# Performance work log

Hardware: AMD Instinct MI355X
Metric: run time of the kernel (lower is better)

Reference implementation:

```python
import jax, jax.numpy as jnp
import numpy as np

HIDDEN = 1024
HEADS = 16
HEAD_DIM = HIDDEN // HEADS
POS_DIM = 128
B, S = 2, 2048
ROPE_BASE = 10000.0


def setup_inputs() -> dict:
    key = jax.random.key(0)
    ks = jax.random.split(key, 8)
    sd = 1.0 / np.sqrt(HIDDEN)
    return {
        "x":   jax.random.normal(ks[0], (B, S, HIDDEN), dtype=jnp.float32),
        "W_q": jax.random.normal(ks[1], (HIDDEN, HIDDEN), dtype=jnp.float32) * sd,
        "W_k": jax.random.normal(ks[2], (HIDDEN, HIDDEN), dtype=jnp.float32) * sd,
        "W_v": jax.random.normal(ks[3], (HIDDEN, HIDDEN), dtype=jnp.float32) * sd,
        "W_o": jax.random.normal(ks[4], (HIDDEN, HIDDEN), dtype=jnp.float32) * sd,
        "repo_W1": jax.random.normal(ks[5], (HIDDEN, POS_DIM), dtype=jnp.float32) * sd,
        "repo_b1": jnp.zeros((POS_DIM,), dtype=jnp.float32),
        "repo_W2": jax.random.normal(ks[6], (POS_DIM, 1), dtype=jnp.float32) * (1.0 / np.sqrt(POS_DIM)),
        "repo_b2": jnp.zeros((1,), dtype=jnp.float32),
    }


def _repo_positions(x, W1, b1, W2, b2):
    # 2-layer MLP -> scalar per token; softplus + cumsum gives monotone learned positions
    h = jax.nn.gelu(jnp.einsum("bsd,dp->bsp", x, W1) + b1)
    raw = (jnp.einsum("bsp,po->bso", h, W2) + b2)[..., 0]      # (B, S)
    return jnp.cumsum(jax.nn.softplus(raw), axis=1)             # (B, S)


def _apply_rope(q, k, positions):
    # q, k: (B, S, H, Dh); positions: (B, S) continuous
    half = HEAD_DIM // 2
    inv_freq = 1.0 / (ROPE_BASE ** (jnp.arange(0, HEAD_DIM, 2, dtype=jnp.float32) / HEAD_DIM))
    angles = positions[:, :, None] * inv_freq                   # (B, S, half)
    cos = jnp.cos(angles)[:, :, None, :]                        # (B, S, 1, half)
    sin = jnp.sin(angles)[:, :, None, :]

    def rot(t):
        t1, t2 = t[..., :half], t[..., half:]
        return jnp.concatenate([t1 * cos - t2 * sin, t1 * sin + t2 * cos], axis=-1)

    return rot(q), rot(k)


def reference(x, W_q, W_k, W_v, W_o, repo_W1, repo_b1, repo_W2, repo_b2):
    scale = 1.0 / np.sqrt(HEAD_DIM)
    q = jnp.einsum("bsd,de->bse", x, W_q).reshape(B, S, HEADS, HEAD_DIM)
    k = jnp.einsum("bsd,de->bse", x, W_k).reshape(B, S, HEADS, HEAD_DIM)
    v = jnp.einsum("bsd,de->bse", x, W_v).reshape(B, S, HEADS, HEAD_DIM)

    positions = _repo_positions(x, repo_W1, repo_b1, repo_W2, repo_b2)
    q, k = _apply_rope(q, k, positions)

    # explicit O(S^2) attention, matching the torch module
    scores = jnp.einsum("bqhd,bkhd->bhqk", q, k) * scale        # (B, H, S, S)
    attn = jax.nn.softmax(scores, axis=-1)
    out = jnp.einsum("bhqk,bkhd->bqhd", attn, v)                # (B, S, H, Dh)
    out = out.reshape(B, S, HIDDEN)
    return jnp.einsum("bsd,de->bse", out, W_o)
```

## Files before the change

### kernel.cpp

```cpp
#include <hip/hip_runtime.h>
#include <hip/hip_bf16.h>
#include <math.h>

#define HIDDEN 1024
#define HEADS 16
#define HEAD_DIM 64
#define POS_DIM 128
#define BATCH 2
#define SEQ 2048
#define TOKENS (BATCH * SEQ)

typedef _Float16 f16;
typedef __attribute__((ext_vector_type(8))) _Float16 f16x8;
typedef __attribute__((ext_vector_type(4))) _Float16 f16x4;
typedef __attribute__((ext_vector_type(4))) float f32x4;

__device__ __forceinline__ void glds16(const f16* g, f16* l) {
    __builtin_amdgcn_global_load_lds((const __attribute__((address_space(1))) unsigned int*)g,
                                     (__attribute__((address_space(3))) unsigned int*)l, 16, 0, 0);
}

__global__ __launch_bounds__(256) void cast_x_kernel(const float* __restrict__ x,
                                                     f16* __restrict__ o) {
    const int i = (blockIdx.x * 256 + threadIdx.x) * 8;
    const float4 u = *(const float4*)(x + i);
    const float4 v = *(const float4*)(x + i + 4);
    f16x8 r = {(f16)u.x, (f16)u.y, (f16)u.z, (f16)u.w,
               (f16)v.x, (f16)v.y, (f16)v.z, (f16)v.w};
    *(f16x8*)(o + i) = r;
}

__global__ __launch_bounds__(256) void cast_wt4_kernel(const float* __restrict__ W0,
                                                       const float* __restrict__ W1,
                                                       const float* __restrict__ W2,
                                                       const float* __restrict__ W3,
                                                       f16* __restrict__ Wt) {
    __shared__ float ts[32][33];
    const int t = threadIdx.x;
    const int z = blockIdx.z;
    const float* W = (z == 0) ? W0 : (z == 1) ? W1 : (z == 2) ? W2 : W3;
    f16* dst = Wt + (size_t)z * HIDDEN * HIDDEN;
    const int k0 = blockIdx.y * 32, n0 = blockIdx.x * 32;
    {
        const int r = t >> 3, c4 = (t & 7) * 4;
        const float4 u = *(const float4*)(W + (size_t)(k0 + r) * HIDDEN + n0 + c4);
        ts[r][c4 + 0] = u.x; ts[r][c4 + 1] = u.y; ts[r][c4 + 2] = u.z; ts[r][c4 + 3] = u.w;
    }
    __syncthreads();
    {
        const int r = t >> 3, c4 = (t & 7) * 4;
        f16* o = dst + (size_t)(n0 + r) * HIDDEN + k0 + c4;
        o[0] = (f16)ts[c4 + 0][r]; o[1] = (f16)ts[c4 + 1][r];
        o[2] = (f16)ts[c4 + 2][r]; o[3] = (f16)ts[c4 + 3][r];
    }
}

__global__ __launch_bounds__(256) void cast_w1t_kernel(const float* __restrict__ W1,
                                                       f16* __restrict__ Wh,
                                                       f16* __restrict__ Wl) {
    __shared__ float ts[32][33];
    const int t = threadIdx.x;
    const int k0 = blockIdx.y * 32, p0 = blockIdx.x * 32;
    {
        const int r = t >> 3, c4 = (t & 7) * 4;
        const float4 u = *(const float4*)(W1 + (size_t)(k0 + r) * POS_DIM + p0 + c4);
        ts[r][c4 + 0] = u.x; ts[r][c4 + 1] = u.y; ts[r][c4 + 2] = u.z; ts[r][c4 + 3] = u.w;
    }
    __syncthreads();
    {
        const int r = t >> 3, c4 = (t & 7) * 4;
        f16* oh = Wh + (size_t)(p0 + r) * HIDDEN + k0 + c4;
        f16* ol = Wl + (size_t)(p0 + r) * HIDDEN + k0 + c4;
#pragma unroll
        for (int u = 0; u < 4; ++u) {
            const float v = ts[c4 + u][r];
            const f16 hi = (f16)v;
            oh[u] = hi;
            ol[u] = (f16)(v - (float)hi);
        }
    }
}

__global__ __launch_bounds__(256, 3) void gemm_gll(const f16* __restrict__ A,
                                                   const f16* __restrict__ Bt,
                                                   f16* __restrict__ Cb,
                                                   float* __restrict__ Cf,
                                                   int N, int f16out) {
    __shared__ __align__(16) f16 As[128 * 64];
    __shared__ __align__(16) f16 Bs[128 * 64];
    const int tid = threadIdx.x;
    const int w = tid >> 6, lane = tid & 63;
    const int g = lane >> 4, c = lane & 15;
    const int m0 = blockIdx.y * 128, n0 = blockIdx.x * 128;
    const int wm = (w & 1) * 64, wn = (w >> 1) * 64;

    const int lrow = lane >> 3;
    const int lseg = (lane & 7) ^ lrow;
    const f16* gA = A + (size_t)(m0 + w * 32 + lrow) * 1024 + lseg * 8;
    const f16* gB = Bt + (size_t)(n0 + w * 32 + lrow) * 1024 + lseg * 8;
    f16* lA = &As[(w * 32) * 64];
    f16* lB = &Bs[(w * 32) * 64];

    f32x4 acc[4][4];
    const f32x4 z = {0.f, 0.f, 0.f, 0.f};
#pragma unroll
    for (int i = 0; i < 4; ++i)
#pragma unroll
        for (int j = 0; j < 4; ++j) acc[i][j] = z;

    const int rsw = c & 7;
    for (int k0 = 0; k0 < 1024; k0 += 64) {
        __syncthreads();
#pragma unroll
        for (int p = 0; p < 4; ++p) {
            glds16(gA + (size_t)p * 8 * 1024 + k0, lA + p * 8 * 64);
            glds16(gB + (size_t)p * 8 * 1024 + k0, lB + p * 8 * 64);
        }
        __syncthreads();
#pragma unroll
        for (int s = 0; s < 2; ++s) {
            f16x8 af[4], bf[4];
#pragma unroll
            for (int i = 0; i < 4; ++i)
                af[i] = *(const f16x8*)&As[(wm + i * 16 + c) * 64 + (((s * 4 + g) ^ rsw) * 8)];
#pragma unroll
            for (int j = 0; j < 4; ++j)
                bf[j] = *(const f16x8*)&Bs[(wn + j * 16 + c) * 64 + (((s * 4 + g) ^ rsw) * 8)];
#pragma unroll
            for (int i = 0; i < 4; ++i)
#pragma unroll
                for (int j = 0; j < 4; ++j)
                    acc[i][j] = __builtin_amdgcn_mfma_f32_16x16x32_f16(af[i], bf[j], acc[i][j], 0, 0, 0);
        }
    }
#pragma unroll
    for (int i = 0; i < 4; ++i)
#pragma unroll
        for (int j = 0; j < 4; ++j)
#pragma unroll
            for (int r = 0; r < 4; ++r) {
                const size_t off = (size_t)(m0 + wm + i * 16 + 4 * g + r) * N + n0 + wn + j * 16 + c;
                if (f16out) Cb[off] = (f16)acc[i][j][r];
                else Cf[off] = acc[i][j][r];
            }
}

__device__ __forceinline__ float gelu_tanh(float x) {
    const float kA = 0.7978845608028654f;
    return 0.5f * x * (1.0f + tanhf(kA * (x + 0.044715f * x * x * x)));
}

__global__ __launch_bounds__(256, 2) void repo_mfma(const float* __restrict__ x,
                                                    const f16* __restrict__ w1h,
                                                    const f16* __restrict__ w1l,
                                                    const float* __restrict__ b1,
                                                    const float* __restrict__ W2,
                                                    const float* __restrict__ b2,
                                                    float* __restrict__ raw) {
    __shared__ __align__(16) f16 Ash[64 * 32], Asl[64 * 32];
    __shared__ __align__(16) f16 Bsh[128 * 32], Bsl[128 * 32];
    __shared__ float red[4][64];
    const int tid = threadIdx.x;
    const int w = tid >> 6, lane = tid & 63;
    const int g = lane >> 4, c = lane & 15;
    const int m0 = blockIdx.x * 64;

    const int arow = tid >> 2, aseg = tid & 3;
    const int aslot = (aseg ^ ((arow ^ (arow >> 2)) & 3)) << 3;
    const float* gA = x + (size_t)(m0 + arow) * 1024 + aseg * 8;
    const f16* gBh0 = w1h + (size_t)arow * 1024 + aseg * 8;
    const f16* gBh1 = w1h + (size_t)(arow + 64) * 1024 + aseg * 8;
    const f16* gBl0 = w1l + (size_t)arow * 1024 + aseg * 8;
    const f16* gBl1 = w1l + (size_t)(arow + 64) * 1024 + aseg * 8;
    f16* sAh = &Ash[arow * 32 + aslot];
    f16* sAl = &Asl[arow * 32 + aslot];
    f16* sBh0 = &Bsh[arow * 32 + aslot];
    f16* sBh1 = &Bsh[(arow + 64) * 32 + aslot];
    f16* sBl0 = &Bsl[arow * 32 + aslot];
    f16* sBl1 = &Bsl[(arow + 64) * 32 + aslot];

    const int foff = ((g ^ ((c ^ (c >> 2)) & 3)) << 3);

    f32x4 acc[4][2];
    const f32x4 z = {0.f, 0.f, 0.f, 0.f};
#pragma unroll
    for (int i = 0; i < 4; ++i) { acc[i][0] = z; acc[i][1] = z; }

    float4 pa0 = *(const float4*)gA;
    float4 pa1 = *(const float4*)(gA + 4);
    f16x8 pbh0 = *(const f16x8*)gBh0, pbh1 = *(const f16x8*)gBh1;
    f16x8 pbl0 = *(const f16x8*)gBl0, pbl1 = *(const f16x8*)gBl1;

    for (int k0 = 0; k0 < 1024; k0 += 32) {
        __syncthreads();
        {
            const float av[8] = {pa0.x, pa0.y, pa0.z, pa0.w, pa1.x, pa1.y, pa1.z, pa1.w};
            f16x8 ah, al;
#pragma unroll
            for (int u = 0; u < 8; ++u) {
                const f16 hi = (f16)av[u];
                ah[u] = hi;
                al[u] = (f16)(av[u] - (float)hi);
            }
            *(f16x8*)sAh = ah; *(f16x8*)sAl = al;
            *(f16x8*)sBh0 = pbh0; *(f16x8*)sBh1 = pbh1;
            *(f16x8*)sBl0 = pbl0; *(f16x8*)sBl1 = pbl1;
        }
        __syncthreads();
        if (k0 + 32 < 1024) {
            pa0 = *(const float4*)(gA + k0 + 32);
            pa1 = *(const float4*)(gA + k0 + 36);
            pbh0 = *(const f16x8*)(gBh0 + k0 + 32);
            pbh1 = *(const f16x8*)(gBh1 + k0 + 32);
            pbl0 = *(const f16x8*)(gBl0 + k0 + 32);
            pbl1 = *(const f16x8*)(gBl1 + k0 + 32);
        }
        f16x8 ah[4], al[4], bh[2], bl[2];
#pragma unroll
        for (int i = 0; i < 4; ++i) {
            ah[i] = *(const f16x8*)&Ash[(i * 16 + c) * 32 + foff];
            al[i] = *(const f16x8*)&Asl[(i * 16 + c) * 32 + foff];
        }
#pragma unroll
        for (int j = 0; j < 2; ++j) {
            bh[j] = *(const f16x8*)&Bsh[(w * 32 + j * 16 + c) * 32 + foff];
            bl[j] = *(const f16x8*)&Bsl[(w * 32 + j * 16 + c) * 32 + foff];
        }
#pragma unroll
        for (int i = 0; i < 4; ++i)
#pragma unroll
            for (int j = 0; j < 2; ++j) {
                acc[i][j] = __builtin_amdgcn_mfma_f32_16x16x32_f16(ah[i], bh[j], acc[i][j], 0, 0, 0);
                acc[i][j] = __builtin_amdgcn_mfma_f32_16x16x32_f16(ah[i], bl[j], acc[i][j], 0, 0, 0);
                acc[i][j] = __builtin_amdgcn_mfma_f32_16x16x32_f16(al[i], bh[j], acc[i][j], 0, 0, 0);
            }
    }
    float b1v[2], w2v[2];
#pragma unroll
    for (int j = 0; j < 2; ++j) {
        const int col = w * 32 + j * 16 + c;
        b1v[j] = b1[col];
        w2v[j] = W2[col];
    }
    float part[4][4];
#pragma unroll
    for (int i = 0; i < 4; ++i)
#pragma unroll
        for (int r = 0; r < 4; ++r) {
            float s = 0.f;
#pragma unroll
            for (int j = 0; j < 2; ++j)
                s += gelu_tanh(acc[i][j][r] + b1v[j]) * w2v[j];
            s += __shfl_xor(s, 1, 64);
            s += __shfl_xor(s, 2, 64);
            s += __shfl_xor(s, 4, 64);
            s += __shfl_xor(s, 8, 64);
            part[i][r] = s;
        }
    if (c == 0)
#pragma unroll
        for (int i = 0; i < 4; ++i)
#pragma unroll
            for (int r = 0; r < 4; ++r)
                red[w][i * 16 + 4 * g + r] = part[i][r];
    __syncthreads();
    if (tid < 64)
        raw[m0 + tid] = red[0][tid] + red[1][tid] + red[2][tid] + red[3][tid] + b2[0];
}

__device__ __forceinline__ double softplus_d(double x) {
    return (x > 0.0) ? x + log1p(exp(-x)) : log1p(exp(x));
}

__global__ __launch_bounds__(256) void repo_cumsum_kernel(const float* __restrict__ raw,
                                                          float* __restrict__ pos) {
    __shared__ double bufA[256];
    __shared__ double bufB[256];
    const int b = blockIdx.x;
    const int t = threadIdx.x;
    const float* r = raw + (size_t)b * SEQ;

    double loc[8];
    double sum = 0.0;
#pragma unroll
    for (int i = 0; i < 8; ++i) {
        sum += softplus_d((double)r[t * 8 + i]);
        loc[i] = sum;
    }
    bufA[t] = sum;
    __syncthreads();

    double* src = bufA;
    double* dst = bufB;
    for (int off = 1; off < 256; off <<= 1) {
        double v = src[t];
        if (t >= off) v += src[t - off];
        dst[t] = v;
        __syncthreads();
        double* tmp = src; src = dst; dst = tmp;
    }
    const double excl = src[t] - sum;
#pragma unroll
    for (int i = 0; i < 8; ++i)
        pos[(size_t)b * SEQ + t * 8 + i] = (float)(excl + loc[i]);
}

__global__ __launch_bounds__(256) void sctab_kernel(const float* __restrict__ pos,
                                                    float* __restrict__ costab,
                                                    float* __restrict__ sintab) {
    const int idx = blockIdx.x * 256 + threadIdx.x;
    const int tok = idx >> 5, i = idx & 31;
    const double ang = (double)pos[tok] * exp(-(double)i * 0.28782313662425574);
    double sa, ca;
    sincos(ang, &sa, &ca);
    costab[idx] = (float)ca;
    sintab[idx] = (float)sa;
}

__global__ __launch_bounds__(256) void packkv_kernel(f16* __restrict__ qkv,
                                                     const float* __restrict__ costab,
                                                     const float* __restrict__ sintab,
                                                     f16* __restrict__ kfo,
                                                     f16* __restrict__ vfo) {
    __shared__ __align__(16) f16 kds[64][72];
    __shared__ __align__(16) f16 vds[64][72];
    const int t = threadIdx.x;
    const int s0 = blockIdx.x * 64;
    const int h = blockIdx.y, b = blockIdx.z;
    const int key = t >> 2, part = t & 3;
    const int tok = b * SEQ + s0 + key;
    {
        float cs[8], sn[8];
        *(float4*)cs       = *(const float4*)(costab + tok * 32 + part * 8);
        *(float4*)(cs + 4) = *(const float4*)(costab + tok * 32 + part * 8 + 4);
        *(float4*)sn       = *(const float4*)(sintab + tok * 32 + part * 8);
        *(float4*)(sn + 4) = *(const float4*)(sintab + tok * 32 + part * 8 + 4);
        f16* qrow = qkv + (size_t)tok * 3072 + h * HEAD_DIM;
        {
            f16x8 lo = *(const f16x8*)(qrow + part * 8);
            f16x8 hi = *(const f16x8*)(qrow + part * 8 + 32);
#pragma unroll
            for (int u = 0; u < 8; ++u) {
                const float l = (float)lo[u], hh = (float)hi[u];
                lo[u] = (f16)(l * cs[u] - hh * sn[u]);
                hi[u] = (f16)(l * sn[u] + hh * cs[u]);
            }
            *(f16x8*)(qrow + part * 8) = lo;
            *(f16x8*)(qrow + part * 8 + 32) = hi;
        }
        const f16* krow = qrow + 1024;
        {
            f16x8 lo = *(const f16x8*)(krow + part * 8);
            f16x8 hi = *(const f16x8*)(krow + part * 8 + 32);
#pragma unroll
            for (int u = 0; u < 8; ++u) {
                const float l = (float)lo[u], hh = (float)hi[u];
                kds[key][part * 8 + u]      = (f16)(l * cs[u] - hh * sn[u]);
                kds[key][32 + part * 8 + u] = (f16)(l * sn[u] + hh * cs[u]);
            }
        }
        const f16* vrow = qrow + 2048;
        f16x8 v0 = *(const f16x8*)(vrow + part * 16);
        f16x8 v1 = *(const f16x8*)(vrow + part * 16 + 8);
#pragma unroll
        for (int u = 0; u < 8; ++u) {
            vds[part * 16 + u][key] = v0[u];
            vds[part * 16 + 8 + u][key] = v1[u];
        }
    }
    __syncthreads();
    const size_t cb = ((size_t)((b * HEADS + h) * 32) + blockIdx.x) * 4096;
#pragma unroll
    for (int p = 0; p < 2; ++p) {
        const int idx = p * 256 + t;
        const int frag = idx >> 6, lane = idx & 63;
        const int jn = frag >> 1, half = frag & 1, g = lane >> 4, c = lane & 15;
        *(f16x8*)(kfo + cb + frag * 512 + lane * 8) =
            *(const f16x8*)(&kds[jn * 16 + c][half * 32 + g * 8]);
    }
#pragma unroll
    for (int p = 0; p < 4; ++p) {
        const int idx = p * 256 + t;
        const int frag = idx >> 6, lane = idx & 63;
        const int jd = frag >> 2, jn = frag & 3, g = lane >> 4, c = lane & 15;
        *(f16x4*)(vfo + cb + frag * 256 + lane * 4) =
            *(const f16x4*)(&vds[jd * 16 + c][jn * 16 + 4 * g]);
    }
}

__global__ __launch_bounds__(256, 2) void attn_f16(const f16* __restrict__ qkv,
                                                   const f16* __restrict__ kfr,
                                                   const f16* __restrict__ vfr,
                                                   f16* __restrict__ aof0,
                                                   f16* __restrict__ aof1,
                                                   float* __restrict__ lsb) {
    __shared__ __align__(16) f16 kls[4096];
    __shared__ __align__(16) f16 vls[4096];
    __shared__ __align__(16) f16 ot[4][32][72];
    const int tid = threadIdx.x;
    const int w = tid >> 6, lane = tid & 63;
    const int g = lane >> 4, c = lane & 15;
    const int h = blockIdx.y;
    const int b = blockIdx.z >> 1, half = blockIdx.z & 1;
    const int bh = b * HEADS + h;
    const int row0 = blockIdx.x * 128 + w * 32;
    const int ch0 = half * 16;

    const f16* qb = qkv + (size_t)(b * SEQ + row0) * 3072 + h * HEAD_DIM + g * 8;
    const f16* kfb = kfr + (size_t)bh * 32 * 4096;
    const f16* vfb = vfr + (size_t)bh * 32 * 4096;

    f16x8 qf[2][2];
#pragma unroll
    for (int i = 0; i < 2; ++i) {
        qf[i][0] = *(const f16x8*)(qb + (size_t)(i * 16 + c) * 3072);
        qf[i][1] = *(const f16x8*)(qb + (size_t)(i * 16 + c) * 3072 + 32);
    }
    const f32x4 z = {0.f, 0.f, 0.f, 0.f};
    f32x4 acc[4][2];
    f32x4 accl[2];
#pragma unroll
    for (int jd = 0; jd < 4; ++jd) { acc[jd][0] = z; acc[jd][1] = z; }
    accl[0] = z; accl[1] = z;

    const f16x4 ones = {(f16)1.f, (f16)1.f, (f16)1.f, (f16)1.f};
    const float SC = 0.125f * 1.4426950408889634f;

    for (int cc = 0; cc < 16; ++cc) {
        const int ch = ch0 + cc;
        __syncthreads();
        {
            const f16* kg = kfb + (size_t)ch * 4096 + w * 1024 + lane * 8;
            const f16* vg = vfb + (size_t)ch * 4096 + w * 1024 + lane * 8;
            glds16(kg, kls + w * 1024);
            glds16(kg + 512, kls + w * 1024 + 512);
            glds16(vg, vls + w * 1024);
            glds16(vg + 512, vls + w * 1024 + 512);
        }
        __syncthreads();

        f16x8 kf[8];
        f16x4 vf[16];
#pragma unroll
        for (int f = 0; f < 8; ++f) kf[f] = *(const f16x8*)(kls + lane * 8 + f * 512);
#pragma unroll
        for (int f = 0; f < 16; ++f) vf[f] = *(const f16x4*)(vls + lane * 4 + f * 256);

#pragma unroll
        for (int i = 0; i < 2; ++i) {
            f32x4 s[4];
#pragma unroll
            for (int jn = 0; jn < 4; ++jn) {
                s[jn] = __builtin_amdgcn_mfma_f32_16x16x32_f16(kf[jn * 2], qf[i][0], z, 0, 0, 0);
                s[jn] = __builtin_amdgcn_mfma_f32_16x16x32_f16(kf[jn * 2 + 1], qf[i][1], s[jn], 0, 0, 0);
            }
#pragma unroll
            for (int jn = 0; jn < 4; ++jn) {
                f16x4 pf;
#pragma unroll
                for (int r = 0; r < 4; ++r)
                    pf[r] = (f16)__builtin_amdgcn_exp2f(fmaf(s[jn][r], SC, -8.0f));
                accl[i] = __builtin_amdgcn_mfma_f32_16x16x16f16(ones, pf, accl[i], 0, 0, 0);
#pragma unroll
                for (int jd = 0; jd < 4; ++jd)
                    acc[jd][i] = __builtin_amdgcn_mfma_f32_16x16x16f16(vf[jd * 4 + jn], pf, acc[jd][i], 0, 0, 0);
            }
        }
    }

    if (lane < 16) {
#pragma unroll
        for (int i = 0; i < 2; ++i)
            lsb[((size_t)(half * 32 + bh)) * SEQ + row0 + i * 16 + lane] = accl[i][0];
    }
#pragma unroll
    for (int i = 0; i < 2; ++i)
#pragma unroll
        for (int jd = 0; jd < 4; ++jd)
#pragma unroll
            for (int r = 0; r < 4; ++r)
                ot[w][i * 16 + c][jd * 16 + 4 * g + r] = (f16)acc[jd][i][r];
    f16* aofH = half ? aof1 : aof0;
    const int tr = lane >> 1, hf = lane & 1;
    f16* aob = aofH + (size_t)(b * SEQ + row0 + tr) * HIDDEN + h * HEAD_DIM + hf * 32;
#pragma unroll
    for (int q = 0; q < 4; ++q)
        *(f16x8*)(aob + q * 8) = *(const f16x8*)(&ot[w][tr][hf * 32 + q * 8]);
}

__global__ __launch_bounds__(256) void combine_kernel(f16* __restrict__ a0,
                                                      const f16* __restrict__ a1,
                                                      const float* __restrict__ lsb) {
    const int idx = blockIdx.x * 256 + threadIdx.x;
    const int part = idx & 127;
    const int tok = idx >> 7;
    const int h = part >> 3, d8 = (part & 7) * 8;
    const int b = tok >> 11, s = tok & 2047;
    const size_t li = (size_t)(b * HEADS + h) * SEQ + s;
    const float inv = 1.0f / (lsb[li] + lsb[32 * SEQ + li]);
    const size_t off = (size_t)tok * HIDDEN + h * HEAD_DIM + d8;
    const f16x8 u = *(const f16x8*)(a0 + off);
    const f16x8 v = *(const f16x8*)(a1 + off);
    f16x8 o;
#pragma unroll
    for (int q = 0; q < 8; ++q) o[q] = (f16)(((float)u[q] + (float)v[q]) * inv);
    *(f16x8*)(a0 + off) = o;
}

extern "C" void kernel_launch(void* const* d_in, const int* in_sizes, int n_in,
                              void* d_out, int out_size, void* d_ws, size_t ws_size,
                              hipStream_t stream) {
    const float* x   = (const float*)d_in[0];
    const float* W_q = (const float*)d_in[1];
    const float* W_k = (const float*)d_in[2];
    const float* W_v = (const float*)d_in[3];
    const float* W_o = (const float*)d_in[4];
    const float* rW1 = (const float*)d_in[5];
    const float* rb1 = (const float*)d_in[6];
    const float* rW2 = (const float*)d_in[7];
    const float* rb2 = (const float*)d_in[8];
    float* out = (float*)d_out;

    const size_t MAT = (size_t)TOKENS * HIDDEN;
    const size_t WSZ = (size_t)HIDDEN * HIDDEN;
    f16* x16  = (f16*)d_ws;
    f16* wqkv = x16 + MAT;
    f16* wot  = wqkv + 3 * WSZ;
    f16* qkv  = wot + WSZ;
    f16* kfr  = qkv + 3 * MAT;
    f16* vfr  = kfr + MAT;
    f16* aof0 = vfr + MAT;
    f16* aof1 = aof0 + MAT;
    f16* w1h  = aof1 + MAT;
    f16* w1l  = w1h + POS_DIM * HIDDEN;
    float* raw    = (float*)(w1l + POS_DIM * HIDDEN);
    float* pos    = raw + TOKENS;
    float* costab = pos + TOKENS;
    float* sintab = costab + TOKENS * 32;
    float* lsb    = sintab + TOKENS * 32;

    cast_x_kernel<<<MAT / 2048, 256, 0, stream>>>(x, x16);
    cast_wt4_kernel<<<dim3(32, 32, 4), 256, 0, stream>>>(W_q, W_k, W_v, W_o, wqkv);
    cast_w1t_kernel<<<dim3(4, 32), 256, 0, stream>>>(rW1, w1h, w1l);

    gemm_gll<<<dim3(24, 32), 256, 0, stream>>>(x16, wqkv, qkv, nullptr, 3072, 1);

    repo_mfma<<<64, 256, 0, stream>>>(x, w1h, w1l, rb1, rW2, rb2, raw);
    repo_cumsum_kernel<<<BATCH, 256, 0, stream>>>(raw, pos);
    sctab_kernel<<<TOKENS * 32 / 256, 256, 0, stream>>>(pos, costab, sintab);

    packkv_kernel<<<dim3(SEQ / 64, HEADS, BATCH), 256, 0, stream>>>(qkv, costab, sintab, kfr, vfr);

    attn_f16<<<dim3(SEQ / 128, HEADS, BATCH * 2), 256, 0, stream>>>(qkv, kfr, vfr, aof0, aof1, lsb);
    combine_kernel<<<TOKENS * 128 / 256, 256, 0, stream>>>(aof0, aof1, lsb);

    gemm_gll<<<dim3(8, 32), 256, 0, stream>>>(aof0, wot, nullptr, out, 1024, 0);
}
```

Baseline: 252.9 us.

## Double-buffer K/V chunk loads in attention and raise occupancy hint

The attention kernel now prefetches the next K/V chunk into an alternate LDS buffer with global_load_lds while computing on the current one. It waits with a partial vmcnt and a raw s_barrier instead of two __syncthreads per iteration. The separate K, V and output LDS arrays are merged into one 32KB region that is reused for the output transpose, and launch_bounds is raised to 4 blocks per CU. This hides global-load latency behind MFMA work, at the cost of more LDS per block and tighter register limits from the higher occupancy target.

```diff
diff --git a/kernel.cpp b/kernel.cpp
--- a/kernel.cpp
+++ b/kernel.cpp
@@ -388,15 +388,13 @@
     }
 }
 
-__global__ __launch_bounds__(256, 2) void attn_f16(const f16* __restrict__ qkv,
+__global__ __launch_bounds__(256, 4) void attn_f16(const f16* __restrict__ qkv,
                                                    const f16* __restrict__ kfr,
                                                    const f16* __restrict__ vfr,
                                                    f16* __restrict__ aof0,
                                                    f16* __restrict__ aof1,
                                                    float* __restrict__ lsb) {
-    __shared__ __align__(16) f16 kls[4096];
-    __shared__ __align__(16) f16 vls[4096];
-    __shared__ __align__(16) f16 ot[4][32][72];
+    __shared__ __align__(16) f16 smem[16384];
     const int tid = threadIdx.x;
     const int w = tid >> 6, lane = tid & 63;
     const int g = lane >> 4, c = lane & 15;
@@ -407,8 +405,8 @@
     const int ch0 = half * 16;
 
     const f16* qb = qkv + (size_t)(b * SEQ + row0) * 3072 + h * HEAD_DIM + g * 8;
-    const f16* kfb = kfr + (size_t)bh * 32 * 4096;
-    const f16* vfb = vfr + (size_t)bh * 32 * 4096;
+    const f16* kfb = kfr + (size_t)bh * 32 * 4096 + (size_t)ch0 * 4096;
+    const f16* vfb = vfr + (size_t)bh * 32 * 4096 + (size_t)ch0 * 4096;
 
     f16x8 qf[2][2];
 #pragma unroll
@@ -426,25 +424,38 @@
     const f16x4 ones = {(f16)1.f, (f16)1.f, (f16)1.f, (f16)1.f};
     const float SC = 0.125f * 1.4426950408889634f;
 
+    {
+        const f16* kg = kfb + w * 1024 + lane * 8;
+        const f16* vg = vfb + w * 1024 + lane * 8;
+        glds16(kg, smem + w * 1024);
+        glds16(kg + 512, smem + w * 1024 + 512);
+        glds16(vg, smem + 8192 + w * 1024);
+        glds16(vg + 512, smem + 8192 + w * 1024 + 512);
+    }
+
     for (int cc = 0; cc < 16; ++cc) {
-        const int ch = ch0 + cc;
-        __syncthreads();
         {
-            const f16* kg = kfb + (size_t)ch * 4096 + w * 1024 + lane * 8;
-            const f16* vg = vfb + (size_t)ch * 4096 + w * 1024 + lane * 8;
-            glds16(kg, kls + w * 1024);
-            glds16(kg + 512, kls + w * 1024 + 512);
-            glds16(vg, vls + w * 1024);
-            glds16(vg + 512, vls + w * 1024 + 512);
-        }
-        __syncthreads();
-
+            const int nc = (cc + 1 < 16) ? cc + 1 : 15;
+            const int nb = (cc + 1) & 1;
+            const f16* kg = kfb + (size_t)nc * 4096 + w * 1024 + lane * 8;
+            const f16* vg = vfb + (size_t)nc * 4096 + w * 1024 + lane * 8;
+            glds16(kg, smem + nb * 4096 + w * 1024);
+            glds16(kg + 512, smem + nb * 4096 + w * 1024 + 512);
+            glds16(vg, smem + 8192 + nb * 4096 + w * 1024);
+            glds16(vg + 512, smem + 8192 + nb * 4096 + w * 1024 + 512);
+        }
+        asm volatile("s_waitcnt vmcnt(4)" ::: "memory");
+        __builtin_amdgcn_s_barrier();
+        asm volatile("" ::: "memory");
+
+        const f16* kb = smem + (cc & 1) * 4096;
+        const f16* vb = smem + 8192 + (cc & 1) * 4096;
         f16x8 kf[8];
         f16x4 vf[16];
 #pragma unroll
-        for (int f = 0; f < 8; ++f) kf[f] = *(const f16x8*)(kls + lane * 8 + f * 512);
-#pragma unroll
-        for (int f = 0; f < 16; ++f) vf[f] = *(const f16x4*)(vls + lane * 4 + f * 256);
+        for (int f = 0; f < 8; ++f) kf[f] = *(const f16x8*)(kb + lane * 8 + f * 512);
+#pragma unroll
+        for (int f = 0; f < 16; ++f) vf[f] = *(const f16x4*)(vb + lane * 4 + f * 256);
 
 #pragma unroll
         for (int i = 0; i < 2; ++i) {
@@ -466,7 +477,10 @@
                     acc[jd][i] = __builtin_amdgcn_mfma_f32_16x16x16f16(vf[jd * 4 + jn], pf, acc[jd][i], 0, 0, 0);
             }
         }
-    }
+        asm volatile("" ::: "memory");
+        __builtin_amdgcn_s_barrier();
+    }
+    __syncthreads();
 
     if (lane < 16) {
 #pragma unroll
@@ -479,13 +493,13 @@
         for (int jd = 0; jd < 4; ++jd)
 #pragma unroll
             for (int r = 0; r < 4; ++r)
-                ot[w][i * 16 + c][jd * 16 + 4 * g + r] = (f16)acc[jd][i][r];
+                smem[(w * 32 + i * 16 + c) * 72 + jd * 16 + 4 * g + r] = (f16)acc[jd][i][r];
     f16* aofH = half ? aof1 : aof0;
     const int tr = lane >> 1, hf = lane & 1;
     f16* aob = aofH + (size_t)(b * SEQ + row0 + tr) * HIDDEN + h * HEAD_DIM + hf * 32;
 #pragma unroll
     for (int q = 0; q < 4; ++q)
-        *(f16x8*)(aob + q * 8) = *(const f16x8*)(&ot[w][tr][hf * 32 + q * 8]);
+        *(f16x8*)(aob + q * 8) = *(const f16x8*)(smem + (w * 32 + tr) * 72 + hf * 32 + q * 8);
 }
 
 __global__ __launch_bounds__(256) void combine_kernel(f16* __restrict__ a0,
```

Result: slower. 264.3 us (+4.5%).
